# Performance work log

Measured on AMD Instinct MI355X. Metric: run time of the kernel, lower is better.

The kernel has to match this reference:

```python
import jax, jax.numpy as jnp
import numpy as np

V = 256   # ascii_max_dim / output vocab
H = 1024  # h_size


def _lstm(x1h, W_ih, W_hh, b_ih, b_hh):
    """Single-layer unidirectional LSTM (PyTorch gate order i,f,g,o).
    x1h: [B,T,V] one-hot inputs; returns hidden states [B,T,H]."""
    B, T, _ = x1h.shape
    # input projection for all timesteps at once: [B,T,4H]
    xg = jnp.einsum('btv,gv->btg', x1h, W_ih) + b_ih + b_hh

    def step(carry, xt):
        h, c = carry
        gates = xt + h @ W_hh.T  # [B,4H]
        i, f, g, o = jnp.split(gates, 4, axis=-1)
        i = jax.nn.sigmoid(i)
        f = jax.nn.sigmoid(f)
        g = jnp.tanh(g)
        o = jax.nn.sigmoid(o)
        c = f * c + i * g
        h = o * jnp.tanh(c)
        return (h, c), h

    h0 = jnp.zeros((B, H), xg.dtype)
    c0 = jnp.zeros((B, H), xg.dtype)
    _, hs = jax.lax.scan(step, (h0, c0), jnp.swapaxes(xg, 0, 1))  # [T,B,H]
    return jnp.swapaxes(hs, 0, 1)  # [B,T,H]


def setup_inputs() -> dict:
    key = jax.random.key(0)
    ks = jax.random.split(key, 8)
    B, T = 8, 2048
    s = 0.05
    return {
        'Xs': jax.random.randint(ks[0], (B, T), 0, V),
        'ys': jax.random.randint(ks[1], (B, T), 0, V),
        'predict': 0,
        'W_ih': jax.random.normal(ks[2], (4 * H, V), dtype=jnp.float32) * s,
        'W_hh': jax.random.normal(ks[3], (4 * H, H), dtype=jnp.float32) * s,
        'b_ih': jax.random.normal(ks[4], (4 * H,), dtype=jnp.float32) * s,
        'b_hh': jax.random.normal(ks[5], (4 * H,), dtype=jnp.float32) * s,
        'W1': jax.random.normal(ks[6], (V, H), dtype=jnp.float32) * s,
        'b1': jax.random.normal(ks[7], (V,), dtype=jnp.float32) * s,
    }


def reference(Xs, ys, predict, W_ih, W_hh, b_ih, b_hh, W1, b1):
    # one-hot encode char ids -> [B,T,V]
    x1h = jax.nn.one_hot(Xs, V, dtype=W_ih.dtype)
    hs = _lstm(x1h, W_ih, W_hh, b_ih, b_hh)            # [B,T,H]
    logits = jnp.einsum('bth,vh->btv', hs, W1) + b1    # [B,T,V]
    if predict:
        prob = jax.nn.softmax(logits, axis=-1)
        return prob, jnp.argmax(prob, axis=-1)
    # CrossEntropyLoss (mean over timesteps) per sequence, averaged over sequences;
    # with equal lengths this is the mean NLL over all (B,T) positions.
    logp = jax.nn.log_softmax(logits, axis=-1)
    nll = -jnp.take_along_axis(logp, ys[..., None], axis=-1).squeeze(-1)
    return jnp.mean(nll)
```

## Files before the change

### kernel.cpp

```cpp
#include <hip/hip_runtime.h>

#define H_  1024
#define B_  8
#define T_  2048
#define V_  256
#define NWG 256
#define NTH 256

__device__ __forceinline__ unsigned agloadu(const unsigned* p) {
  return __hip_atomic_load(p, __ATOMIC_RELAXED, __HIP_MEMORY_SCOPE_AGENT);
}
__device__ __forceinline__ void agstoreu(unsigned* p, unsigned v) {
  __hip_atomic_store(p, v, __ATOMIC_RELAXED, __HIP_MEMORY_SCOPE_AGENT);
}
__device__ __forceinline__ unsigned f2bf_hi(float f) {
  unsigned u = __builtin_bit_cast(unsigned, f);
  return (u + 0x7fffu + ((u >> 16) & 1u)) & 0xffff0000u;
}
__device__ __forceinline__ float bf_hi2f(unsigned w) {
  return __builtin_bit_cast(float, w & 0xffff0000u);
}

__global__ __launch_bounds__(NTH, 1)
void charrnn_lstm(const int* __restrict__ Xs, const int* __restrict__ ys,
                  const float* __restrict__ W_ih, const float* __restrict__ W_hh,
                  const float* __restrict__ b_ih, const float* __restrict__ b_hh,
                  const float* __restrict__ W1, const float* __restrict__ b1,
                  float* __restrict__ out, unsigned* __restrict__ hgw)
{
  __shared__ float hstage[B_][H_];
  __shared__ float Wis[16][V_];
  __shared__ float stash[H_];
  __shared__ float logits_s[V_];
  __shared__ float gates_s[16][8];
  __shared__ float c_s[4][8];
  __shared__ float bias_s[16];
  __shared__ int   xw[8][32];

  const int wg   = blockIdx.x;
  const int tid  = threadIdx.x;
  const int b_g  = wg & 7;
  const int slot = wg >> 3;
  const int row  = tid >> 4;
  const int seg  = tid & 15;

  const int rg = (row >> 2) * H_ + wg * 4 + (row & 3);
  float4 wreg[16];
  #pragma unroll
  for (int q = 0; q < 16; ++q)
    wreg[q] = *(const float4*)&W_hh[(size_t)rg * H_ + seg * 4 + q * 64];

  for (int i = tid; i < 16 * (V_ / 4); i += NTH) {
    int rl = i >> 6;
    int kq = i & 63;
    int rr = (rl >> 2) * H_ + wg * 4 + (rl & 3);
    *(float4*)&Wis[rl][kq * 4] = *(const float4*)&W_ih[(size_t)rr * V_ + kq * 4];
  }
  if (tid < 16) {
    int rr = (tid >> 2) * H_ + wg * 4 + (tid & 3);
    bias_s[tid] = b_ih[rr] + b_hh[rr];
  }
  if (tid < 32) c_s[tid >> 3][tid & 7] = 0.f;

  int   pending = 0, chunk = 0, ptau = 0;
  float wg_loss = 0.f;

  auto do_chunk = [&]() {
    const int v_loc = tid >> 5, lane32 = tid & 31;
    const int vg = chunk * 8 + v_loc;
    const float* wrow = &W1[(size_t)vg * H_];
    float4 la = make_float4(0.f, 0.f, 0.f, 0.f);
    #pragma unroll
    for (int j = 0; j < 8; ++j) {
      const int k0 = lane32 * 4 + j * 128;
      const float4 w4 = *(const float4*)&wrow[k0];
      const float4 h4 = *(const float4*)&stash[k0];
      la.x = fmaf(w4.x, h4.x, la.x);
      la.y = fmaf(w4.y, h4.y, la.y);
      la.z = fmaf(w4.z, h4.z, la.z);
      la.w = fmaf(w4.w, h4.w, la.w);
    }
    float l = (la.x + la.y) + (la.z + la.w);
    #pragma unroll
    for (int m = 1; m < 32; m <<= 1) l += __shfl_xor(l, m, 64);
    if (lane32 == 0) logits_s[vg] = l + b1[vg];
    chunk++;
    if (chunk == 32) {
      __syncthreads();
      if (tid < 64) {
        float mx = -3.4e38f;
        #pragma unroll
        for (int i2 = 0; i2 < 4; ++i2) mx = fmaxf(mx, logits_s[tid * 4 + i2]);
        #pragma unroll
        for (int m = 1; m < 64; m <<= 1) mx = fmaxf(mx, __shfl_xor(mx, m, 64));
        float se = 0.f;
        #pragma unroll
        for (int i2 = 0; i2 < 4; ++i2) se += __expf(logits_s[tid * 4 + i2] - mx);
        #pragma unroll
        for (int m = 1; m < 64; m <<= 1) se += __shfl_xor(se, m, 64);
        if (tid == 0) {
          const float ly = logits_s[ys[b_g * T_ + ptau]];
          wg_loss += -(ly - mx - __logf(se));
        }
      }
      pending = 0;
      chunk = 0;
      __syncthreads();
    }
  };

  __syncthreads();

  for (int t = 0; t < T_; ++t) {
    const unsigned* hb = hgw + (size_t)((t + 1) & 1) * (B_ * H_);
    const unsigned tag = (unsigned)t;
    unsigned v[32];
    for (;;) {
      bool ok = true;
      #pragma unroll
      for (int i = 0; i < 32; ++i) v[i] = agloadu(&hb[i * NTH + tid]);
      #pragma unroll
      for (int i = 0; i < 32; ++i) ok &= ((v[i] & 0xffffu) == tag);
      if (ok) break;
      __builtin_amdgcn_s_sleep(1);
    }
    #pragma unroll
    for (int i = 0; i < 32; ++i) {
      const int idx = i * NTH + tid;
      hstage[idx >> 10][idx & (H_ - 1)] = bf_hi2f(v[i]);
    }
    if ((t & 31) == 0) {
      const int b = tid >> 5, tt = t + (tid & 31);
      xw[b][tid & 31] = (tt < T_) ? Xs[b * T_ + tt] : 0;
    }
    __syncthreads();

    float4 acc[8];
    #pragma unroll
    for (int b = 0; b < 8; ++b) acc[b] = make_float4(0.f, 0.f, 0.f, 0.f);
    #pragma unroll
    for (int q = 0; q < 16; ++q) {
      const int k0 = seg * 4 + q * 64;
      const float4 w = wreg[q];
      #pragma unroll
      for (int b = 0; b < 8; ++b) {
        const float4 h4 = *(const float4*)&hstage[b][k0];
        acc[b].x = fmaf(w.x, h4.x, acc[b].x);
        acc[b].y = fmaf(w.y, h4.y, acc[b].y);
        acc[b].z = fmaf(w.z, h4.z, acc[b].z);
        acc[b].w = fmaf(w.w, h4.w, acc[b].w);
      }
    }
    float s[8];
    #pragma unroll
    for (int b = 0; b < 8; ++b) s[b] = (acc[b].x + acc[b].y) + (acc[b].z + acc[b].w);
    #pragma unroll
    for (int m = 1; m < 16; m <<= 1) {
      #pragma unroll
      for (int b = 0; b < 8; ++b) s[b] += __shfl_xor(s[b], m, 64);
    }
    if (seg < 8)
      gates_s[row][seg] = s[seg] + Wis[row][xw[seg][t & 31]] + bias_s[row];
    __syncthreads();

    if (tid < 32) {
      const int jj = tid >> 3, b = tid & 7;
      float iv = gates_s[jj][b],      fv = gates_s[4 + jj][b];
      float gv = gates_s[8 + jj][b],  ov = gates_s[12 + jj][b];
      iv = 1.f / (1.f + __expf(-iv));
      fv = 1.f / (1.f + __expf(-fv));
      gv = tanhf(gv);
      ov = 1.f / (1.f + __expf(-ov));
      const float c = fv * c_s[jj][b] + iv * gv;
      c_s[jj][b] = c;
      const float h = ov * tanhf(c);
      agstoreu(&hgw[(size_t)(t & 1) * (B_ * H_) + b * H_ + wg * 4 + jj],
               f2bf_hi(h) | (unsigned)(t + 1));
    }

    const int tau = t - 1;
    const bool newst = (tau >= 0 && (tau & 31) == slot && !pending);
    if (newst) {
      for (int i = tid; i < H_; i += NTH) stash[i] = hstage[b_g][i];
    }
    if (newst) { pending = 1; chunk = 0; ptau = tau; }
    __syncthreads();

    if (pending) do_chunk();
  }

  while (pending) do_chunk();

  if (slot == 31) {
    const unsigned* hb = hgw + (size_t)((T_ - 1) & 1) * (B_ * H_);
    for (int k = 0; k < H_ / NTH; ++k) {
      const int i = k * NTH + tid;
      unsigned w;
      do { w = agloadu(&hb[b_g * H_ + i]); } while ((w & 0xffffu) != (unsigned)T_);
      stash[i] = bf_hi2f(w);
    }
    pending = 1; chunk = 0; ptau = T_ - 1;
    __syncthreads();
    while (pending) do_chunk();
  }

  if (tid == 0) atomicAdd(out, wg_loss * (1.0f / (B_ * T_)));
}

extern "C" void kernel_launch(void* const* d_in, const int* in_sizes, int n_in,
                              void* d_out, int out_size, void* d_ws, size_t ws_size,
                              hipStream_t stream) {
  const int*   Xs   = (const int*)d_in[0];
  const int*   ys   = (const int*)d_in[1];
  const float* W_ih = (const float*)d_in[3];
  const float* W_hh = (const float*)d_in[4];
  const float* b_ih = (const float*)d_in[5];
  const float* b_hh = (const float*)d_in[6];
  const float* W1   = (const float*)d_in[7];
  const float* b1   = (const float*)d_in[8];
  float* out = (float*)d_out;

  unsigned* hgw = (unsigned*)d_ws;

  hipMemsetAsync(d_out, 0, sizeof(float) * (size_t)out_size, stream);
  hipMemsetAsync(d_ws, 0, 2 * B_ * H_ * sizeof(unsigned), stream);

  void* args[] = { (void*)&Xs, (void*)&ys, (void*)&W_ih, (void*)&W_hh,
                   (void*)&b_ih, (void*)&b_hh, (void*)&W1, (void*)&b1,
                   (void*)&out, (void*)&hgw };
  hipError_t e = hipLaunchCooperativeKernel((const void*)charrnn_lstm, dim3(NWG),
                                            dim3(NTH), args, 0, stream);
  if (e != hipSuccess) {
    hipLaunchKernelGGL(charrnn_lstm, dim3(NWG), dim3(NTH), 0, stream,
                       Xs, ys, W_ih, W_hh, b_ih, b_hh, W1, b1, out, hgw);
  }
}
```

Measured before the change: 9.916 ms.

## Pack two bf16 hidden values per 64-bit flagged word and retile matvec 2 rows x 4 batches

The hidden-state exchange buffer now stores two bf16 values plus a 32-bit step tag in each 64-bit atomic word. This halves the number of polled global loads per step and the number of flag stores. The recurrent matvec is retiled so each thread holds two W_hh rows and handles four batch entries. That halves the LDS h reads per FMA, but doubles the weight registers to 128 floats per thread, which raises register pressure.

```diff
diff --git a/kernel.cpp b/kernel.cpp
--- a/kernel.cpp
+++ b/kernel.cpp
@@ -7,18 +7,20 @@
 #define NWG 256
 #define NTH 256
 
-__device__ __forceinline__ unsigned agloadu(const unsigned* p) {
+typedef unsigned long long u64;
+
+__device__ __forceinline__ u64 agload64(const u64* p) {
   return __hip_atomic_load(p, __ATOMIC_RELAXED, __HIP_MEMORY_SCOPE_AGENT);
 }
-__device__ __forceinline__ void agstoreu(unsigned* p, unsigned v) {
+__device__ __forceinline__ void agstore64(u64* p, u64 v) {
   __hip_atomic_store(p, v, __ATOMIC_RELAXED, __HIP_MEMORY_SCOPE_AGENT);
 }
-__device__ __forceinline__ unsigned f2bf_hi(float f) {
+__device__ __forceinline__ unsigned f2bf(float f) {
   unsigned u = __builtin_bit_cast(unsigned, f);
-  return (u + 0x7fffu + ((u >> 16) & 1u)) & 0xffff0000u;
-}
-__device__ __forceinline__ float bf_hi2f(unsigned w) {
-  return __builtin_bit_cast(float, w & 0xffff0000u);
+  return (u + 0x7fffu + ((u >> 16) & 1u)) >> 16;
+}
+__device__ __forceinline__ float bf2f(unsigned hw) {
+  return __builtin_bit_cast(float, hw << 16);
 }
 
 __global__ __launch_bounds__(NTH, 1)
@@ -26,7 +28,7 @@
                   const float* __restrict__ W_ih, const float* __restrict__ W_hh,
                   const float* __restrict__ b_ih, const float* __restrict__ b_hh,
                   const float* __restrict__ W1, const float* __restrict__ b1,
-                  float* __restrict__ out, unsigned* __restrict__ hgw)
+                  float* __restrict__ out, u64* __restrict__ hg64)
 {
   __shared__ float hstage[B_][H_];
   __shared__ float Wis[16][V_];
@@ -41,14 +43,19 @@
   const int tid  = threadIdx.x;
   const int b_g  = wg & 7;
   const int slot = wg >> 3;
-  const int row  = tid >> 4;
   const int seg  = tid & 15;
-
-  const int rg = (row >> 2) * H_ + wg * 4 + (row & 3);
-  float4 wreg[16];
+  const int bh   = (tid >> 4) & 1;
+  const int rp   = tid >> 5;
+
+  const int r0 = rp * 2, r1 = r0 + 1;
+  const int rg0 = (r0 >> 2) * H_ + wg * 4 + (r0 & 3);
+  const int rg1 = (r1 >> 2) * H_ + wg * 4 + (r1 & 3);
+  float4 wreg[2][16];
   #pragma unroll
-  for (int q = 0; q < 16; ++q)
-    wreg[q] = *(const float4*)&W_hh[(size_t)rg * H_ + seg * 4 + q * 64];
+  for (int q = 0; q < 16; ++q) {
+    wreg[0][q] = *(const float4*)&W_hh[(size_t)rg0 * H_ + seg * 4 + q * 64];
+    wreg[1][q] = *(const float4*)&W_hh[(size_t)rg1 * H_ + seg * 4 + q * 64];
+  }
 
   for (int i = tid; i < 16 * (V_ / 4); i += NTH) {
     int rl = i >> 6;
@@ -112,22 +119,25 @@
   __syncthreads();
 
   for (int t = 0; t < T_; ++t) {
-    const unsigned* hb = hgw + (size_t)((t + 1) & 1) * (B_ * H_);
+    const u64* hb = hg64 + (size_t)((t + 1) & 1) * (B_ * H_ / 2);
     const unsigned tag = (unsigned)t;
-    unsigned v[32];
+    u64 v[16];
     for (;;) {
       bool ok = true;
       #pragma unroll
-      for (int i = 0; i < 32; ++i) v[i] = agloadu(&hb[i * NTH + tid]);
-      #pragma unroll
-      for (int i = 0; i < 32; ++i) ok &= ((v[i] & 0xffffu) == tag);
+      for (int i = 0; i < 16; ++i) v[i] = agload64(&hb[i * NTH + tid]);
+      #pragma unroll
+      for (int i = 0; i < 16; ++i) ok &= ((unsigned)v[i] == tag);
       if (ok) break;
       __builtin_amdgcn_s_sleep(1);
     }
     #pragma unroll
-    for (int i = 0; i < 32; ++i) {
+    for (int i = 0; i < 16; ++i) {
       const int idx = i * NTH + tid;
-      hstage[idx >> 10][idx & (H_ - 1)] = bf_hi2f(v[i]);
+      const int b = idx >> 9, p = idx & 511;
+      *(float2*)&hstage[b][p * 2] =
+          make_float2(bf2f((unsigned)(v[i] >> 32) & 0xffffu),
+                      bf2f((unsigned)(v[i] >> 48)));
     }
     if ((t & 31) == 0) {
       const int b = tid >> 5, tt = t + (tid & 31);
@@ -135,32 +145,47 @@
     }
     __syncthreads();
 
-    float4 acc[8];
-    #pragma unroll
-    for (int b = 0; b < 8; ++b) acc[b] = make_float4(0.f, 0.f, 0.f, 0.f);
+    float4 acc[2][4];
+    #pragma unroll
+    for (int r2 = 0; r2 < 2; ++r2)
+      #pragma unroll
+      for (int bb = 0; bb < 4; ++bb) acc[r2][bb] = make_float4(0.f, 0.f, 0.f, 0.f);
     #pragma unroll
     for (int q = 0; q < 16; ++q) {
       const int k0 = seg * 4 + q * 64;
-      const float4 w = wreg[q];
-      #pragma unroll
-      for (int b = 0; b < 8; ++b) {
-        const float4 h4 = *(const float4*)&hstage[b][k0];
-        acc[b].x = fmaf(w.x, h4.x, acc[b].x);
-        acc[b].y = fmaf(w.y, h4.y, acc[b].y);
-        acc[b].z = fmaf(w.z, h4.z, acc[b].z);
-        acc[b].w = fmaf(w.w, h4.w, acc[b].w);
+      float4 h4[4];
+      #pragma unroll
+      for (int bb = 0; bb < 4; ++bb) h4[bb] = *(const float4*)&hstage[bh * 4 + bb][k0];
+      #pragma unroll
+      for (int r2 = 0; r2 < 2; ++r2) {
+        const float4 w = wreg[r2][q];
+        #pragma unroll
+        for (int bb = 0; bb < 4; ++bb) {
+          acc[r2][bb].x = fmaf(w.x, h4[bb].x, acc[r2][bb].x);
+          acc[r2][bb].y = fmaf(w.y, h4[bb].y, acc[r2][bb].y);
+          acc[r2][bb].z = fmaf(w.z, h4[bb].z, acc[r2][bb].z);
+          acc[r2][bb].w = fmaf(w.w, h4[bb].w, acc[r2][bb].w);
+        }
       }
     }
-    float s[8];
-    #pragma unroll
-    for (int b = 0; b < 8; ++b) s[b] = (acc[b].x + acc[b].y) + (acc[b].z + acc[b].w);
+    float s[2][4];
+    #pragma unroll
+    for (int r2 = 0; r2 < 2; ++r2)
+      #pragma unroll
+      for (int bb = 0; bb < 4; ++bb)
+        s[r2][bb] = (acc[r2][bb].x + acc[r2][bb].y) + (acc[r2][bb].z + acc[r2][bb].w);
     #pragma unroll
     for (int m = 1; m < 16; m <<= 1) {
       #pragma unroll
-      for (int b = 0; b < 8; ++b) s[b] += __shfl_xor(s[b], m, 64);
-    }
-    if (seg < 8)
-      gates_s[row][seg] = s[seg] + Wis[row][xw[seg][t & 31]] + bias_s[row];
+      for (int r2 = 0; r2 < 2; ++r2)
+        #pragma unroll
+        for (int bb = 0; bb < 4; ++bb) s[r2][bb] += __shfl_xor(s[r2][bb], m, 64);
+    }
+    if (seg < 8) {
+      const int r2 = seg >> 2, bb = seg & 3;
+      const int r = rp * 2 + r2, b = bh * 4 + bb;
+      gates_s[r][b] = s[r2][bb] + Wis[r][xw[b][t & 31]] + bias_s[r];
+    }
     __syncthreads();
 
     if (tid < 32) {
@@ -174,8 +199,13 @@
       const float c = fv * c_s[jj][b] + iv * gv;
       c_s[jj][b] = c;
       const float h = ov * tanhf(c);
-      agstoreu(&hgw[(size_t)(t & 1) * (B_ * H_) + b * H_ + wg * 4 + jj],
-               f2bf_hi(h) | (unsigned)(t + 1));
+      const unsigned hb16 = f2bf(h);
+      const unsigned ph = (unsigned)__shfl_xor((int)hb16, 8, 64);
+      if ((jj & 1) == 0) {
+        const u64 w = ((u64)ph << 48) | ((u64)hb16 << 32) | (unsigned)(t + 1);
+        agstore64(&hg64[(size_t)(t & 1) * (B_ * H_ / 2) + b * (H_ / 2)
+                        + wg * 2 + (jj >> 1)], w);
+      }
     }
 
     const int tau = t - 1;
@@ -192,12 +222,13 @@
   while (pending) do_chunk();
 
   if (slot == 31) {
-    const unsigned* hb = hgw + (size_t)((T_ - 1) & 1) * (B_ * H_);
-    for (int k = 0; k < H_ / NTH; ++k) {
-      const int i = k * NTH + tid;
-      unsigned w;
-      do { w = agloadu(&hb[b_g * H_ + i]); } while ((w & 0xffffu) != (unsigned)T_);
-      stash[i] = bf_hi2f(w);
+    const u64* hb = hg64 + (size_t)((T_ - 1) & 1) * (B_ * H_ / 2);
+    for (int k = 0; k < 2; ++k) {
+      const int p = k * NTH + tid;
+      u64 w;
+      do { w = agload64(&hb[b_g * (H_ / 2) + p]); } while ((unsigned)w != (unsigned)T_);
+      *(float2*)&stash[p * 2] = make_float2(bf2f((unsigned)(w >> 32) & 0xffffu),
+                                            bf2f((unsigned)(w >> 48)));
     }
     pending = 1; chunk = 0; ptau = T_ - 1;
     __syncthreads();
@@ -220,18 +251,18 @@
   const float* b1   = (const float*)d_in[8];
   float* out = (float*)d_out;
 
-  unsigned* hgw = (unsigned*)d_ws;
+  u64* hg64 = (u64*)d_ws;
 
   hipMemsetAsync(d_out, 0, sizeof(float) * (size_t)out_size, stream);
-  hipMemsetAsync(d_ws, 0, 2 * B_ * H_ * sizeof(unsigned), stream);
+  hipMemsetAsync(d_ws, 0, 2 * (B_ * H_ / 2) * sizeof(u64), stream);
 
   void* args[] = { (void*)&Xs, (void*)&ys, (void*)&W_ih, (void*)&W_hh,
                    (void*)&b_ih, (void*)&b_hh, (void*)&W1, (void*)&b1,
-                   (void*)&out, (void*)&hgw };
+                   (void*)&out, (void*)&hg64 };
   hipError_t e = hipLaunchCooperativeKernel((const void*)charrnn_lstm, dim3(NWG),
                                             dim3(NTH), args, 0, stream);
   if (e != hipSuccess) {
     hipLaunchKernelGGL(charrnn_lstm, dim3(NWG), dim3(NTH), 0, stream,
-                       Xs, ys, W_ih, W_hh, b_ih, b_hh, W1, b1, out, hgw);
-  }
-}
+                       Xs, ys, W_ih, W_hh, b_ih, b_hh, W1, b1, out, hg64);
+  }
+}
```

Measured after the change: 16.34 ms. 1.65x slower.

## Pack four bf16 hidden values per 64-bit atomic word with 2-bit step tag

Applied to the files above, without the earlier changes.

Hidden-state exchange between workgroups now packs four bf16 values into one 64-bit word, with a 2-bit step tag stolen from the low mantissa bits of the first value. This replaces per-element 32-bit words carrying a 16-bit tag. Each thread polls 8 loads per step instead of 32, and each workgroup writes 8 stores instead of 32, cutting global traffic and polling cost on the critical recurrence path. The trade-off is that one in four hidden values loses two mantissa bits, and the shortened tag relies on the double buffering plus the per-step barrier to avoid aliasing.

```diff
diff --git a/kernel.cpp b/kernel.cpp
--- a/kernel.cpp
+++ b/kernel.cpp
@@ -6,19 +6,23 @@
 #define V_  256
 #define NWG 256
 #define NTH 256
-
-__device__ __forceinline__ unsigned agloadu(const unsigned* p) {
+#define WPS (B_ * H_ / 4)
+
+typedef unsigned long long u64;
+
+__device__ __forceinline__ u64 agload64(const u64* p) {
   return __hip_atomic_load(p, __ATOMIC_RELAXED, __HIP_MEMORY_SCOPE_AGENT);
 }
-__device__ __forceinline__ void agstoreu(unsigned* p, unsigned v) {
+__device__ __forceinline__ void agstore64(u64* p, u64 v) {
   __hip_atomic_store(p, v, __ATOMIC_RELAXED, __HIP_MEMORY_SCOPE_AGENT);
 }
-__device__ __forceinline__ unsigned f2bf_hi(float f) {
+__device__ __forceinline__ unsigned f2bf(float f) {
   unsigned u = __builtin_bit_cast(unsigned, f);
-  return (u + 0x7fffu + ((u >> 16) & 1u)) & 0xffff0000u;
-}
-__device__ __forceinline__ float bf_hi2f(unsigned w) {
-  return __builtin_bit_cast(float, w & 0xffff0000u);
+  return (u + 0x7fffu + ((u >> 16) & 1u)) >> 16;
+}
+__device__ __forceinline__ unsigned f2bf14(float f) {
+  unsigned u = __builtin_bit_cast(unsigned, f);
+  return ((u + 0x1FFFFu + ((u >> 18) & 1u)) >> 18) << 2;
 }
 
 __global__ __launch_bounds__(NTH, 1)
@@ -26,7 +30,7 @@
                   const float* __restrict__ W_ih, const float* __restrict__ W_hh,
                   const float* __restrict__ b_ih, const float* __restrict__ b_hh,
                   const float* __restrict__ W1, const float* __restrict__ b1,
-                  float* __restrict__ out, unsigned* __restrict__ hgw)
+                  float* __restrict__ out, u64* __restrict__ hg64)
 {
   __shared__ float hstage[B_][H_];
   __shared__ float Wis[16][V_];
@@ -112,22 +116,27 @@
   __syncthreads();
 
   for (int t = 0; t < T_; ++t) {
-    const unsigned* hb = hgw + (size_t)((t + 1) & 1) * (B_ * H_);
-    const unsigned tag = (unsigned)t;
-    unsigned v[32];
+    const u64* hb = hg64 + (size_t)((t + 1) & 1) * WPS;
+    const unsigned tagp = (unsigned)t & 3u;
+    u64 v[8];
     for (;;) {
       bool ok = true;
       #pragma unroll
-      for (int i = 0; i < 32; ++i) v[i] = agloadu(&hb[i * NTH + tid]);
-      #pragma unroll
-      for (int i = 0; i < 32; ++i) ok &= ((v[i] & 0xffffu) == tag);
+      for (int i = 0; i < 8; ++i) v[i] = agload64(&hb[i * NTH + tid]);
+      #pragma unroll
+      for (int i = 0; i < 8; ++i) ok &= (((unsigned)v[i] & 3u) == tagp);
       if (ok) break;
       __builtin_amdgcn_s_sleep(1);
     }
     #pragma unroll
-    for (int i = 0; i < 32; ++i) {
-      const int idx = i * NTH + tid;
-      hstage[idx >> 10][idx & (H_ - 1)] = bf_hi2f(v[i]);
+    for (int i = 0; i < 8; ++i) {
+      const unsigned lo = (unsigned)v[i], hi = (unsigned)(v[i] >> 32);
+      float4 f;
+      f.x = __builtin_bit_cast(float, (lo & 0xFFFCu) << 16);
+      f.y = __builtin_bit_cast(float, lo & 0xFFFF0000u);
+      f.z = __builtin_bit_cast(float, (hi & 0xFFFFu) << 16);
+      f.w = __builtin_bit_cast(float, hi & 0xFFFF0000u);
+      *(float4*)&hstage[i][tid * 4] = f;
     }
     if ((t & 31) == 0) {
       const int b = tid >> 5, tt = t + (tid & 31);
@@ -174,8 +183,16 @@
       const float c = fv * c_s[jj][b] + iv * gv;
       c_s[jj][b] = c;
       const float h = ov * tanhf(c);
-      agstoreu(&hgw[(size_t)(t & 1) * (B_ * H_) + b * H_ + wg * 4 + jj],
-               f2bf_hi(h) | (unsigned)(t + 1));
+      const unsigned full = f2bf(h);
+      const unsigned tagd = f2bf14(h) | ((unsigned)(t + 1) & 3u);
+      const unsigned r16 = (jj == 0) ? tagd : full;
+      const unsigned p1 = (unsigned)__shfl((int)r16, b + 8, 64);
+      const unsigned p2 = (unsigned)__shfl((int)r16, b + 16, 64);
+      const unsigned p3 = (unsigned)__shfl((int)r16, b + 24, 64);
+      if (tid < 8) {
+        const u64 w = (u64)r16 | ((u64)p1 << 16) | ((u64)p2 << 32) | ((u64)p3 << 48);
+        agstore64(&hg64[(size_t)(t & 1) * WPS + tid * 256 + wg], w);
+      }
     }
 
     const int tau = t - 1;
@@ -192,13 +209,17 @@
   while (pending) do_chunk();
 
   if (slot == 31) {
-    const unsigned* hb = hgw + (size_t)((T_ - 1) & 1) * (B_ * H_);
-    for (int k = 0; k < H_ / NTH; ++k) {
-      const int i = k * NTH + tid;
-      unsigned w;
-      do { w = agloadu(&hb[b_g * H_ + i]); } while ((w & 0xffffu) != (unsigned)T_);
-      stash[i] = bf_hi2f(w);
-    }
+    const u64* hb = hg64 + (size_t)((T_ - 1) & 1) * WPS;
+    u64 w;
+    do { w = agload64(&hb[b_g * 256 + tid]); }
+    while (((unsigned)w & 3u) != ((unsigned)T_ & 3u));
+    const unsigned lo = (unsigned)w, hi = (unsigned)(w >> 32);
+    float4 f;
+    f.x = __builtin_bit_cast(float, (lo & 0xFFFCu) << 16);
+    f.y = __builtin_bit_cast(float, lo & 0xFFFF0000u);
+    f.z = __builtin_bit_cast(float, (hi & 0xFFFFu) << 16);
+    f.w = __builtin_bit_cast(float, hi & 0xFFFF0000u);
+    *(float4*)&stash[tid * 4] = f;
     pending = 1; chunk = 0; ptau = T_ - 1;
     __syncthreads();
     while (pending) do_chunk();
@@ -220,18 +241,18 @@
   const float* b1   = (const float*)d_in[8];
   float* out = (float*)d_out;
 
-  unsigned* hgw = (unsigned*)d_ws;
+  u64* hg64 = (u64*)d_ws;
 
   hipMemsetAsync(d_out, 0, sizeof(float) * (size_t)out_size, stream);
-  hipMemsetAsync(d_ws, 0, 2 * B_ * H_ * sizeof(unsigned), stream);
+  hipMemsetAsync(d_ws, 0, 2 * WPS * sizeof(u64), stream);
 
   void* args[] = { (void*)&Xs, (void*)&ys, (void*)&W_ih, (void*)&W_hh,
                    (void*)&b_ih, (void*)&b_hh, (void*)&W1, (void*)&b1,
-                   (void*)&out, (void*)&hgw };
+                   (void*)&out, (void*)&hg64 };
   hipError_t e = hipLaunchCooperativeKernel((const void*)charrnn_lstm, dim3(NWG),
                                             dim3(NTH), args, 0, stream);
   if (e != hipSuccess) {
     hipLaunchKernelGGL(charrnn_lstm, dim3(NWG), dim3(NTH), 0, stream,
-                       Xs, ys, W_ih, W_hh, b_ih, b_hh, W1, b1, out, hgw);
-  }
-}
+                       Xs, ys, W_ih, W_hh, b_ih, b_hh, W1, b1, out, hg64);
+  }
+}
```

After: 9.308 ms. -6.1%, faster.
